# Kernel optimization log

Hardware: AMD Instinct MI355X
Metric: run time of the kernel (lower is better)

## Reference

```python
import jax, jax.numpy as jnp
import numpy as np

B, V, T, C, HIN, WIN = 1, 6, 3, 256, 32, 32
NH = 8
LN_EPS = 1e-5


def setup_inputs() -> dict:
    key = jax.random.key(0)
    ks = jax.random.split(key, 14)
    s = 0.02
    lim = 1.0 / np.sqrt(C)
    def lin_w(k):
        return jax.random.uniform(k, (C, C), jnp.float32, -lim, lim)
    return {
        "history_feats": jax.random.normal(ks[0], (B, V, T, C, HIN, WIN), jnp.float32),
        "query_embed": jax.random.normal(ks[1], (1, C, 1, 1), jnp.float32) * s,
        "camera_pos_embed": jax.random.normal(ks[2], (V, C), jnp.float32) * s,
        "temporal_pos_embed": jax.random.normal(ks[3], (T, C), jnp.float32) * s,
        "spatial_pos_embed": jax.random.normal(ks[4], (1, C, 1, 1), jnp.float32) * s,
        "q_w": lin_w(ks[5]), "q_b": jnp.zeros((C,), jnp.float32),
        "k_w": lin_w(ks[6]), "k_b": jnp.zeros((C,), jnp.float32),
        "v_w": lin_w(ks[7]), "v_b": jnp.zeros((C,), jnp.float32),
        "o_w": lin_w(ks[8]), "o_b": jnp.zeros((C,), jnp.float32),
        "ln_g": jnp.ones((C,), jnp.float32),
        "ln_b": jnp.zeros((C,), jnp.float32),
        "query_cam_idx": 0,
        "H": 32,
        "W": 32,
    }


def reference(history_feats, query_embed, camera_pos_embed, temporal_pos_embed,
              spatial_pos_embed, q_w, q_b, k_w, k_b, v_w, v_b, o_w, o_b,
              ln_g, ln_b, query_cam_idx, H, W):
    B_, V_, T_, C_, Hin, Win = history_feats.shape
    dh = C_ // NH
    # --- build query: [B, H*W, C] ---
    q = query_embed + camera_pos_embed[query_cam_idx][None, :, None, None] + spatial_pos_embed
    q = jnp.broadcast_to(q, (B_, C_, H, W)).reshape(B_, C_, H * W).transpose(0, 2, 1)
    kv = (history_feats
          + temporal_pos_embed[None, None, :, :, None, None]
          + camera_pos_embed[None, :, None, :, None, None])
    kv = kv.transpose(0, 1, 2, 4, 5, 3).reshape(B_, V_ * T_ * Hin * Win, C_)
    # --- projections (torch Linear: x @ W.T + b) ---
    qp = q @ q_w.T + q_b
    kp = kv @ k_w.T + k_b
    vp = kv @ v_w.T + v_b
    # --- split heads: [B, NH, L, dh] ---
    qh = qp.reshape(B_, H * W, NH, dh).transpose(0, 2, 1, 3)
    kh = kp.reshape(B_, -1, NH, dh).transpose(0, 2, 1, 3)
    vh = vp.reshape(B_, -1, NH, dh).transpose(0, 2, 1, 3)
    scale = float(dh) ** -0.5
    attn = jax.nn.softmax(jnp.einsum('bhqd,bhkd->bhqk', qh, kh) * scale, axis=-1)
    out = jnp.einsum('bhqk,bhkd->bhqd', attn, vh)
    out = out.transpose(0, 2, 1, 3).reshape(B_, H * W, C_)
    out = out @ o_w.T + o_b
    # --- LayerNorm over channel dim ---
    mu = out.mean(-1, keepdims=True)
    var = ((out - mu) ** 2).mean(-1, keepdims=True)
    out = (out - mu) * jax.lax.rsqrt(var + LN_EPS) * ln_g + ln_b
    return out.transpose(0, 2, 1).reshape(B_, C_, H, W)
```

## Files before the change

kernel.cpp:

```cpp
#include <hip/hip_runtime.h>
#include <hip/hip_fp16.h>

typedef const float* fcp;

#define C_    256
#define NH_   8
#define DH_   32
#define VT_   18
#define HWK   1024
#define L_    (VT_*HWK)
#define SCALE_ 0.17677669529663687f

#define EMB_OFF  0
#define WF_OFF   4608
#define BB_OFF   6656
#define PSVT_OFF 6720
#define CTX_OFF  6912
#define Y_OFF    8960
#define Z_OFF    9216

__device__ __forceinline__ float blockReduceSum256(float v){
  __shared__ float red[4];
  #pragma unroll
  for (int off = 32; off; off >>= 1) v += __shfl_xor(v, off, 64);
  const int lane = threadIdx.x & 63, w = threadIdx.x >> 6;
  __syncthreads();
  if (lane == 0) red[w] = v;
  __syncthreads();
  return red[0] + red[1] + red[2] + red[3];
}

__global__ void k_fold(fcp qe, fcp cam, fcp tpe, fcp spe, const int* __restrict__ cidx,
                       fcp qw, fcp qb, fcp kw, fcp kb, float* __restrict__ ws){
  __shared__ float qvS[C_];
  __shared__ float qpS[DH_];
  const int b = blockIdx.x, t = threadIdx.x, lane = t & 63, wv = t >> 6;
  const int ci = cidx[0];
  qvS[t] = qe[t] + cam[ci*C_ + t] + spe[t];
  {
    const int v = b/3, tt = b - v*3;
    ws[EMB_OFF + b*C_ + t] = tpe[tt*C_ + t] + cam[v*C_ + t];
  }
  if (b == 8){
    #pragma unroll
    for (int i = 0; i < 8; i++) ws[CTX_OFF + i*256 + t] = 0.f;
    if (t < 144) ws[PSVT_OFF + t] = 0.f;
  }
  __syncthreads();
  if (b < 8){
    #pragma unroll
    for (int i = 0; i < 8; i++){
      const int r = b*DH_ + wv*8 + i;
      fcp qr = qw + (size_t)r*C_;
      float v = qr[lane]*qvS[lane] + qr[64+lane]*qvS[64+lane]
              + qr[128+lane]*qvS[128+lane] + qr[192+lane]*qvS[192+lane];
      #pragma unroll
      for (int off = 32; off; off >>= 1) v += __shfl_xor(v, off, 64);
      if (lane == 0) qpS[wv*8 + i] = v + qb[r];
    }
    __syncthreads();
    float acc = 0.f;
    #pragma unroll 8
    for (int d = 0; d < DH_; d++)
      acc += qpS[d] * kw[(size_t)(b*DH_ + d)*C_ + t];
    ws[WF_OFF + b*C_ + t] = SCALE_ * acc;
    if (t == 0){
      float bb = 0.f;
      for (int d = 0; d < DH_; d++) bb += qpS[d] * kb[b*DH_ + d];
      ws[BB_OFF + b] = SCALE_ * bb;
    }
  }
}

__global__ void k_attn(fcp feats, float* __restrict__ ws){
  __shared__ __align__(16) float wf[C_*8];
  __shared__ float redS[32];
  __shared__ float basef[8];
  __shared__ __align__(16) float pred[8*512];
  __shared__ float pexS[64*8];
  __shared__ __align__(16) __half fS[8*32*66];
  const int bid = blockIdx.x, vt = bid >> 4, sc = bid & 15, t = threadIdx.x;

  for (int idx = t; idx < 2048; idx += 512){
    const int h = idx >> 8, c = idx & 255;
    wf[c*8 + h] = ws[WF_OFF + idx];
  }
  __syncthreads();
  if (t < 256){
    const float e = ws[EMB_OFF + vt*C_ + t];
    const float4 wa = *(const float4*)&wf[t*8];
    const float4 wb = *(const float4*)&wf[t*8 + 4];
    float pb[8] = {e*wa.x, e*wa.y, e*wa.z, e*wa.w, e*wb.x, e*wb.y, e*wb.z, e*wb.w};
    #pragma unroll
    for (int h = 0; h < 8; h++){
      float v = pb[h];
      #pragma unroll
      for (int off = 32; off; off >>= 1) v += __shfl_xor(v, off, 64);
      if ((t & 63) == 0) redS[(t >> 6)*8 + h] = v;
    }
  }
  __syncthreads();
  if (t < 8) basef[t] = redS[t] + redS[8+t] + redS[16+t] + redS[24+t] + ws[BB_OFF + t];
  __syncthreads();
  const int s = t & 63, cg = t >> 6;
  fcp fp = feats + ((size_t)vt*C_ + cg*32)*HWK + sc*64 + s;
  float acc[8] = {0,0,0,0,0,0,0,0};
  #pragma unroll 8
  for (int i = 0; i < 32; i++){
    const float fv = fp[(size_t)i*HWK];
    fS[(cg*32 + i)*66 + s] = __float2half(fv);
    const float4 wa = *(const float4*)&wf[(cg*32+i)*8];
    const float4 wb = *(const float4*)&wf[(cg*32+i)*8 + 4];
    acc[0] += fv*wa.x; acc[1] += fv*wa.y; acc[2] += fv*wa.z; acc[3] += fv*wa.w;
    acc[4] += fv*wb.x; acc[5] += fv*wb.y; acc[6] += fv*wb.z; acc[7] += fv*wb.w;
  }
  #pragma unroll
  for (int h = 0; h < 8; h++) pred[cg*512 + h*64 + s] = acc[h];
  __syncthreads();
  {
    const int h1 = t >> 6, tok = t & 63;
    float sum = basef[h1];
    #pragma unroll
    for (int cg2 = 0; cg2 < 8; cg2++) sum += pred[cg2*512 + t];
    const float e = __expf(sum);
    pexS[tok*8 + h1] = e;
    float v = e;
    #pragma unroll
    for (int off = 32; off; off >>= 1) v += __shfl_xor(v, off, 64);
    if (tok == 0) atomicAdd(&ws[PSVT_OFF + vt*8 + h1], v);
  }
  __syncthreads();
  const int lane = t & 63, hB = lane & 7, isub = lane >> 3;
  float aB[4] = {0.f, 0.f, 0.f, 0.f};
  #pragma unroll 4
  for (int s2 = 0; s2 < 64; s2 += 2){
    const float pe0 = pexS[s2*8 + hB];
    const float pe1 = pexS[s2*8 + 8 + hB];
    #pragma unroll
    for (int p = 0; p < 4; p++){
      const __half2 h2 = *(const __half2*)&fS[(cg*32 + p*8 + isub)*66 + s2];
      const float2 f2 = __half22float2(h2);
      aB[p] += pe0 * f2.x + pe1 * f2.y;
    }
  }
  #pragma unroll
  for (int p = 0; p < 4; p++)
    atomicAdd(&ws[CTX_OFF + hB*256 + cg*32 + p*8 + isub], aB[p]);
}

__global__ void k_vproj(fcp vw, fcp vb, float* __restrict__ ws){
  __shared__ float psS[144];
  const int r = blockIdx.x, t = threadIdx.x, h = r >> 5;
  if (t < 144) psS[t] = ws[PSVT_OFF + t];
  __syncthreads();
  float denom = 0.f, embP = 0.f;
  #pragma unroll
  for (int vt = 0; vt < VT_; vt++){
    const float P = psS[vt*8 + h];
    denom += P;
    embP  += ws[EMB_OFF + vt*C_ + t] * P;
  }
  const float ctx = ws[CTX_OFF + h*256 + t];
  const float ctxn = (ctx + embP) / denom;
  float v = vw[(size_t)r*C_ + t] * ctxn;
  v = blockReduceSum256(v);
  if (t == 0) ws[Y_OFF + r] = v + vb[r];
}

__global__ void k_oproj(fcp ow, fcp ob, float* __restrict__ ws){
  const int r = blockIdx.x, t = threadIdx.x;
  float v = ow[(size_t)r*C_ + t] * ws[Y_OFF + t];
  v = blockReduceSum256(v);
  if (t == 0) ws[Z_OFF + r] = v + ob[r];
}

__global__ void k_out(fcp lng, fcp lnb, const float* __restrict__ ws,
                      float* __restrict__ out, int hw){
  const int c = blockIdx.x, t = threadIdx.x;
  const float z = ws[Z_OFF + t];
  const float s  = blockReduceSum256(z);
  const float s2 = blockReduceSum256(z*z);
  const float mu = s * (1.f/C_);
  const float var = s2 * (1.f/C_) - mu*mu;
  const float rs = rsqrtf(var + 1e-5f);
  const float fin = (ws[Z_OFF + c] - mu) * rs * lng[c] + lnb[c];
  float4 pk = make_float4(fin, fin, fin, fin);
  ((float4*)(out + (size_t)c*hw))[t] = pk;
}

extern "C" void kernel_launch(void* const* d_in, const int* in_sizes, int n_in,
                              void* d_out, int out_size, void* d_ws, size_t ws_size,
                              hipStream_t stream) {
  fcp feats = (fcp)d_in[0];
  fcp qe    = (fcp)d_in[1];
  fcp cam   = (fcp)d_in[2];
  fcp tpe   = (fcp)d_in[3];
  fcp spe   = (fcp)d_in[4];
  fcp qw    = (fcp)d_in[5];
  fcp qb    = (fcp)d_in[6];
  fcp kw    = (fcp)d_in[7];
  fcp kb    = (fcp)d_in[8];
  fcp vw    = (fcp)d_in[9];
  fcp vb    = (fcp)d_in[10];
  fcp ow    = (fcp)d_in[11];
  fcp ob    = (fcp)d_in[12];
  fcp lng   = (fcp)d_in[13];
  fcp lnb   = (fcp)d_in[14];
  const int* cidx = (const int*)d_in[15];
  float* ws = (float*)d_ws;
  float* out = (float*)d_out;
  const int hw = out_size / C_;

  k_fold  <<<18,  256, 0, stream>>>(qe, cam, tpe, spe, cidx, qw, qb, kw, kb, ws);
  k_attn  <<<288, 512, 0, stream>>>(feats, ws);
  k_vproj <<<256, 256, 0, stream>>>(vw, vb, ws);
  k_oproj <<<256, 256, 0, stream>>>(ow, ob, ws);
  k_out   <<<256, 256, 0, stream>>>(lng, lnb, ws, out, hw);
}
```

Before: 137.2 us.

## Split context atomics per view-time slot and preload feature column into registers

Global context accumulation is split into 18 per-(view,time) partial buffers, which cuts atomic contention from 288 blocks onto one 2048-float buffer down to 16 blocks per slot. k_vproj then sums the 18 partials. In the attention kernel, the 32 feature loads are issued up front into registers so more memory requests are in flight. The eight-way shared-memory partial-score buffer is replaced by shared atomics into a single 512-float array, trading a smaller shared footprint and simpler reduction for LDS atomic cost and higher register pressure.

```diff
diff --git a/kernel.cpp b/kernel.cpp
--- a/kernel.cpp
+++ b/kernel.cpp
@@ -15,9 +15,9 @@
 #define WF_OFF   4608
 #define BB_OFF   6656
 #define PSVT_OFF 6720
-#define CTX_OFF  6912
-#define Y_OFF    8960
-#define Z_OFF    9216
+#define Y_OFF    6912
+#define Z_OFF    7168
+#define CTXP_OFF 7424
 
 __device__ __forceinline__ float blockReduceSum256(float v){
   __shared__ float red[4];
@@ -41,10 +41,10 @@
     const int v = b/3, tt = b - v*3;
     ws[EMB_OFF + b*C_ + t] = tpe[tt*C_ + t] + cam[v*C_ + t];
   }
-  if (b == 8){
-    #pragma unroll
-    for (int i = 0; i < 8; i++) ws[CTX_OFF + i*256 + t] = 0.f;
-    if (t < 144) ws[PSVT_OFF + t] = 0.f;
+  {
+    #pragma unroll
+    for (int i = 0; i < 8; i++) ws[CTXP_OFF + b*2048 + i*256 + t] = 0.f;
+    if (b == 8 && t < 144) ws[PSVT_OFF + t] = 0.f;
   }
   __syncthreads();
   if (b < 8){
@@ -76,11 +76,12 @@
   __shared__ __align__(16) float wf[C_*8];
   __shared__ float redS[32];
   __shared__ float basef[8];
-  __shared__ __align__(16) float pred[8*512];
+  __shared__ float predS[512];
   __shared__ float pexS[64*8];
   __shared__ __align__(16) __half fS[8*32*66];
   const int bid = blockIdx.x, vt = bid >> 4, sc = bid & 15, t = threadIdx.x;
 
+  predS[t] = 0.f;
   for (int idx = t; idx < 2048; idx += 512){
     const int h = idx >> 8, c = idx & 255;
     wf[c*8 + h] = ws[WF_OFF + idx];
@@ -104,24 +105,25 @@
   __syncthreads();
   const int s = t & 63, cg = t >> 6;
   fcp fp = feats + ((size_t)vt*C_ + cg*32)*HWK + sc*64 + s;
+  float fv[32];
+  #pragma unroll
+  for (int i = 0; i < 32; i++) fv[i] = fp[(size_t)i*HWK];
   float acc[8] = {0,0,0,0,0,0,0,0};
-  #pragma unroll 8
+  #pragma unroll
   for (int i = 0; i < 32; i++){
-    const float fv = fp[(size_t)i*HWK];
-    fS[(cg*32 + i)*66 + s] = __float2half(fv);
+    fS[(cg*32 + i)*66 + s] = __float2half(fv[i]);
     const float4 wa = *(const float4*)&wf[(cg*32+i)*8];
     const float4 wb = *(const float4*)&wf[(cg*32+i)*8 + 4];
-    acc[0] += fv*wa.x; acc[1] += fv*wa.y; acc[2] += fv*wa.z; acc[3] += fv*wa.w;
-    acc[4] += fv*wb.x; acc[5] += fv*wb.y; acc[6] += fv*wb.z; acc[7] += fv*wb.w;
-  }
-  #pragma unroll
-  for (int h = 0; h < 8; h++) pred[cg*512 + h*64 + s] = acc[h];
+    acc[0] += fv[i]*wa.x; acc[1] += fv[i]*wa.y; acc[2] += fv[i]*wa.z; acc[3] += fv[i]*wa.w;
+    acc[4] += fv[i]*wb.x; acc[5] += fv[i]*wb.y; acc[6] += fv[i]*wb.z; acc[7] += fv[i]*wb.w;
+  }
+  #pragma unroll
+  for (int h = 0; h < 8; h++)
+    atomicAdd(&predS[h*64 + s], acc[h]);
   __syncthreads();
   {
     const int h1 = t >> 6, tok = t & 63;
-    float sum = basef[h1];
-    #pragma unroll
-    for (int cg2 = 0; cg2 < 8; cg2++) sum += pred[cg2*512 + t];
+    const float sum = basef[h1] + predS[t];
     const float e = __expf(sum);
     pexS[tok*8 + h1] = e;
     float v = e;
@@ -145,7 +147,7 @@
   }
   #pragma unroll
   for (int p = 0; p < 4; p++)
-    atomicAdd(&ws[CTX_OFF + hB*256 + cg*32 + p*8 + isub], aB[p]);
+    atomicAdd(&ws[CTXP_OFF + vt*2048 + hB*256 + cg*32 + p*8 + isub], aB[p]);
 }
 
 __global__ void k_vproj(fcp vw, fcp vb, float* __restrict__ ws){
@@ -153,14 +155,14 @@
   const int r = blockIdx.x, t = threadIdx.x, h = r >> 5;
   if (t < 144) psS[t] = ws[PSVT_OFF + t];
   __syncthreads();
-  float denom = 0.f, embP = 0.f;
+  float denom = 0.f, embP = 0.f, ctx = 0.f;
   #pragma unroll
   for (int vt = 0; vt < VT_; vt++){
     const float P = psS[vt*8 + h];
     denom += P;
     embP  += ws[EMB_OFF + vt*C_ + t] * P;
-  }
-  const float ctx = ws[CTX_OFF + h*256 + t];
+    ctx   += ws[CTXP_OFF + vt*2048 + h*256 + t];
+  }
   const float ctxn = (ctx + embP) / denom;
   float v = vw[(size_t)r*C_ + t] * ctxn;
   v = blockReduceSum256(v);
```

Result: faster. 134.5 us, median of 3 (-2.0%).
